# Performance work log

Measured on AMD Instinct MI355X. Metric: run time of the kernel, lower is better.

Reference implementation:

```python
import jax, jax.numpy as jnp
import numpy as np

N = 100000
E = 1600000
F_IN, HID, N_CLS = 128, 16, 32


def setup_inputs() -> dict:
    key = jax.random.key(0)
    ks = jax.random.split(key, 10)
    x = jax.random.normal(ks[0], (N, F_IN), dtype=jnp.float32)
    edge_index = jax.random.randint(ks[1], (2, E), 0, N, dtype=jnp.int64)
    edge_weight = jax.random.uniform(ks[2], (E,), dtype=jnp.float32)
    def glorot(k, shape):
        lim = np.sqrt(6.0 / (shape[0] + shape[1])).astype(np.float32)
        return jax.random.uniform(k, shape, dtype=jnp.float32, minval=-lim, maxval=lim)
    return {
        'x': x, 'edge_index': edge_index, 'edge_weight': edge_weight,
        'W1_0': glorot(ks[3], (F_IN, HID)), 'W1_1': glorot(ks[4], (F_IN, HID)),
        'b1': jnp.zeros((HID,), jnp.float32),
        'W2_0': glorot(ks[5], (HID, N_CLS)), 'W2_1': glorot(ks[6], (HID, N_CLS)),
        'b2': jnp.zeros((N_CLS,), jnp.float32),
    }


def _cheb_conv_k2(x, row, col, edge_weight, W0, W1, b):
    # PyG ChebConv, K=2, lambda_max=2.0:
    #   T0 = x; T1 = L_hat x = D^{-1/2} A D^{-1/2} x - x
    n = x.shape[0]
    deg = jax.ops.segment_sum(edge_weight, row, num_segments=n)  # [N]
    dinv = jnp.where(deg > 0, jax.lax.rsqrt(deg), 0.0)
    norm = dinv[row] * edge_weight * dinv[col]                   # [E]
    agg = jax.ops.segment_sum(norm[:, None] * x[col], row, num_segments=n)  # [N,F]
    tx1 = agg - x
    return x @ W0 + tx1 @ W1 + b


def reference(x, edge_index, edge_weight, W1_0, W1_1, b1, W2_0, W2_1, b2):
    row, col = edge_index[0], edge_index[1]
    h = jax.nn.relu(_cheb_conv_k2(x, row, col, edge_weight, W1_0, W1_1, b1))
    # dropout(p=0) and DFA layers are identity in forward
    out = _cheb_conv_k2(h, row, col, edge_weight, W2_0, W2_1, b2)
    return jax.nn.log_softmax(out, axis=1)
```

## Files before the change

kernel.cpp:

```cpp
#include <hip/hip_runtime.h>
#include <hip/hip_bf16.h>


#include <hip/hip_fp16.h>

constexpr int NN   = 100000;
constexpr int NE   = 1600000;
constexpr int FIN  = 128;
constexpr int HID  = 16;
constexpr int NCLS = 32;

constexpr int RB    = 256;
constexpr int NBKT  = (NN + RB - 1) / RB;
constexpr int EPB   = 4096;
constexpr int EPT   = EPB / 256;
constexpr int GP    = (NE + EPB - 1) / EPB;
constexpr int CAP   = 8192;
constexpr int NTILE = NN / 16;
constexpr int NPAIR = NN / 2;

typedef float f32x2 __attribute__((ext_vector_type(2)));
typedef float f32x4 __attribute__((ext_vector_type(4)));
typedef short bf16x8 __attribute__((ext_vector_type(8)));

#if defined(__has_builtin)
#if __has_builtin(__builtin_amdgcn_cvt_pk_f32_fp8)
#define HAVE_CVT_FP8 1
#endif
#endif

static __device__ __forceinline__ unsigned int f2e4m3(float f) {
    union { float f; unsigned int u; } v; v.f = f;
    unsigned int s = (v.u >> 24) & 0x80u;
    unsigned int au = v.u & 0x7fffffffu;
    if (au > 0x43E00000u) au = 0x43E00000u;
    au += 0x7ffffu + ((au >> 20) & 1u);
    int e4 = (int)(au >> 23) - 120;
    unsigned int m = (au >> 20) & 7u;
    unsigned int byte = (e4 <= 0) ? 0u : (((unsigned int)e4 << 3) | m);
    return s | byte;
}
static __device__ __forceinline__ void fp8x4_fma(unsigned int v, float w, float* acc) {
#ifdef HAVE_CVT_FP8
    f32x2 lo = __builtin_amdgcn_cvt_pk_f32_fp8((int)v, false);
    f32x2 hi = __builtin_amdgcn_cvt_pk_f32_fp8((int)v, true);
    acc[0] += w * lo.x; acc[1] += w * lo.y;
    acc[2] += w * hi.x; acc[3] += w * hi.y;
#else
#pragma unroll
    for (int i = 0; i < 4; i++) {
        unsigned int b = (v >> (8 * i)) & 0xffu;
        float f = __int_as_float((int)(((b & 0x80u) << 24) | ((b & 0x7fu) << 20))) * 0x1p120f;
        acc[i] += w * f;
    }
#endif
}
static __device__ __forceinline__ unsigned short f2bf(float f) {
    union { float f; unsigned int u; } v; v.f = f;
    unsigned int r = v.u + 0x7fffu + ((v.u >> 16) & 1u);
    return (unsigned short)(r >> 16);
}
static __device__ __forceinline__ float bf2f(unsigned short b) {
    union { unsigned int u; float f; } v; v.u = ((unsigned int)b) << 16;
    return v.f;
}
static __device__ __forceinline__ unsigned int wpack(float wf) {
    unsigned int b = __float_as_uint(wf) + 0x8000u;
    return (b >> 16) & 0x7fffu;
}
static __device__ __forceinline__ float wdec(unsigned int u) {
    return __uint_as_float((u >> 17) << 16);
}

__global__ void k_zero_cur(int* __restrict__ bucketCursor) {
    int i = blockIdx.x * blockDim.x + threadIdx.x;
    if (i < NBKT) bucketCursor[i] = 0;
}

__global__ __launch_bounds__(256) void k_partition(
    const int* __restrict__ row, const int* __restrict__ col,
    const float* __restrict__ w, int* __restrict__ bucketCursor,
    int2* __restrict__ partS) {
    __shared__ int2 stage[EPB];
    __shared__ unsigned short sbkt[EPB];
    __shared__ int cnt[NBKT];
    __shared__ int lofs[NBKT];
    __shared__ int cursor[NBKT];
    __shared__ int gbase[NBKT];
    __shared__ int sa[512], sb[512];
    int tid = threadIdx.x;
    long ebase = (long)blockIdx.x * EPB;
    int rr[EPT]; int cc[EPT]; float wv[EPT];
#pragma unroll
    for (int i = 0; i < EPT; i++) {
        long e = ebase + i * 256 + tid;
        if (e < NE) { rr[i] = row[e]; cc[i] = col[e]; wv[i] = w[e]; }
        else rr[i] = -1;
    }
    for (int i = tid; i < NBKT; i += 256) cnt[i] = 0;
    __syncthreads();
#pragma unroll
    for (int i = 0; i < EPT; i++)
        if (rr[i] >= 0) atomicAdd(&cnt[rr[i] >> 8], 1);
    __syncthreads();
    for (int i = tid; i < 512; i += 256) sa[i] = (i < NBKT) ? cnt[i] : 0;
    __syncthreads();
    int* src = sa; int* dst = sb;
    for (int off = 1; off < 512; off <<= 1) {
        for (int i = tid; i < 512; i += 256)
            dst[i] = src[i] + ((i >= off) ? src[i - off] : 0);
        __syncthreads();
        int* t = src; src = dst; dst = t;
    }
    for (int i = tid; i < NBKT; i += 256) {
        int ex = src[i] - cnt[i];
        lofs[i] = ex;
        cursor[i] = ex;
        int go = (cnt[i] > 0) ? atomicAdd(&bucketCursor[i], cnt[i]) : 0;
        gbase[i] = i * CAP + go;
    }
    __syncthreads();
#pragma unroll
    for (int i = 0; i < EPT; i++) {
        if (rr[i] >= 0) {
            int b = rr[i] >> 8;
            int p = atomicAdd(&cursor[b], 1);
            int2 v;
            v.x = cc[i] | ((rr[i] & 255) << 17);
            v.y = __float_as_int(wv[i]);
            stage[p] = v;
            sbkt[p] = (unsigned short)b;
        }
    }
    __syncthreads();
    int total = (int)min((long)EPB, NE - ebase);
    for (int i = tid; i < total; i += 256) {
        int b = sbkt[i];
        partS[gbase[b] + (i - lofs[b])] = stage[i];
    }
}

__global__ __launch_bounds__(256) void k_bucket_sort(
    const int2* __restrict__ partS, const int* __restrict__ bucketCursor,
    unsigned int* __restrict__ partC, int* __restrict__ rowptr,
    float* __restrict__ dinv) {
    __shared__ int hist[RB];
    __shared__ int cursor[RB];
    __shared__ float dsum[RB];
    __shared__ int wtot[4];
    __shared__ int red[4];
    int b = blockIdx.x;
    int tid = threadIdx.x;
    int lane = tid & 63, wv = tid >> 6;
    int partial = 0;
    for (int i = tid; i < b; i += 256) partial += bucketCursor[i];
#pragma unroll
    for (int off = 1; off < 64; off <<= 1) partial += __shfl_xor(partial, off, 64);
    if (lane == 0) red[wv] = partial;
    hist[tid] = 0;
    dsum[tid] = 0.f;
    __syncthreads();
    int start = red[0] + red[1] + red[2] + red[3];
    int count = bucketCursor[b];
    const int2* src = partS + (long)b * CAP;
    for (int i = tid; i < count; i += 256)
        atomicAdd(&hist[((unsigned)src[i].x >> 17) & 255], 1);
    __syncthreads();
    int v = hist[tid];
    int sc = v;
#pragma unroll
    for (int off = 1; off < 64; off <<= 1) {
        int up = __shfl_up(sc, off, 64);
        if (lane >= off) sc += up;
    }
    if (lane == 63) wtot[wv] = sc;
    __syncthreads();
    int add = 0;
    for (int w2 = 0; w2 < wv; w2++) add += wtot[w2];
    int ex = sc + add - v;
    int node = b * RB + tid;
    if (node <= NN) rowptr[node] = start + ex;
    cursor[tid] = ex;
    __syncthreads();
    for (int i = tid; i < count; i += 256) {
        int2 p = src[i];
        int rl = ((unsigned)p.x >> 17) & 255;
        int pos = atomicAdd(&cursor[rl], 1);
        float wf = __int_as_float(p.y);
        partC[start + pos] = ((unsigned)p.x & 0x1FFFFu) | (wpack(wf) << 17);
        atomicAdd(&dsum[rl], wf);
    }
    __syncthreads();
    if (node < NN) {
        float dsv = dsum[tid];
        dinv[node] = dsv > 0.f ? rsqrtf(dsv) : 0.f;
    }
}

__global__ __launch_bounds__(256) void k_proj1(
    const float* __restrict__ x, const float* __restrict__ W0,
    const float* __restrict__ W1, const float* __restrict__ b1,
    const float* __restrict__ dinv,
    float* __restrict__ xa, unsigned char* __restrict__ xb8) {
    int wid = (int)(((long)blockIdx.x * 256 + threadIdx.x) >> 6);
    if (wid >= NTILE) return;
    int lane = threadIdx.x & 63;
    int col = lane & 15, quad = lane >> 4;

    bf16x8 bfrag[2][4];
#pragma unroll
    for (int mat = 0; mat < 2; mat++) {
        const float* W = mat ? W1 : W0;
#pragma unroll
        for (int kb = 0; kb < 4; kb++) {
            bf16x8 f;
#pragma unroll
            for (int j = 0; j < 8; j++)
                f[j] = (short)f2bf(W[(kb * 32 + quad * 8 + j) * HID + col]);
            bfrag[mat][kb] = f;
        }
    }

    const float* xrow = x + ((long)wid * 16 + col) * FIN + quad * 8;
    float4 xb[8];
#pragma unroll
    for (int kb = 0; kb < 4; kb++) {
        xb[2 * kb]     = *(const float4*)(xrow + kb * 32);
        xb[2 * kb + 1] = *(const float4*)(xrow + kb * 32 + 4);
    }
    f32x4 acc0 = {0.f, 0.f, 0.f, 0.f}, acc1 = {0.f, 0.f, 0.f, 0.f};
#pragma unroll
    for (int kb = 0; kb < 4; kb++) {
        float4 a0 = xb[2 * kb], a1 = xb[2 * kb + 1];
        bf16x8 af;
        af[0] = (short)f2bf(a0.x); af[1] = (short)f2bf(a0.y);
        af[2] = (short)f2bf(a0.z); af[3] = (short)f2bf(a0.w);
        af[4] = (short)f2bf(a1.x); af[5] = (short)f2bf(a1.y);
        af[6] = (short)f2bf(a1.z); af[7] = (short)f2bf(a1.w);
        acc0 = __builtin_amdgcn_mfma_f32_16x16x32_bf16(af, bfrag[0][kb], acc0, 0, 0, 0);
        acc1 = __builtin_amdgcn_mfma_f32_16x16x32_bf16(af, bfrag[1][kb], acc1, 0, 0, 0);
    }

    float b1v = b1[col];
#pragma unroll
    for (int r = 0; r < 4; r++) {
        long node = (long)wid * 16 + quad * 4 + r;
        float a0 = acc0[r], a1 = acc1[r];
        xa[node * HID + col] = a0 - a1 + b1v;
        float dn = dinv[node];
        xb8[node * HID + col] = (unsigned char)f2e4m3(dn * a1);
    }
}

__global__ __launch_bounds__(256) void k_gather1(
    const int* __restrict__ rowptr, const unsigned int* __restrict__ partC,
    const float* __restrict__ dinv, const unsigned char* __restrict__ xb8,
    const float* __restrict__ xa,
    unsigned short* __restrict__ h16, unsigned char* __restrict__ h8) {
    long t = (long)blockIdx.x * 256 + threadIdx.x;
    int w = (int)(t >> 6);
    if (w >= NPAIR) return;
    int lane = threadIdx.x & 63;
    int d = lane & 3, p = lane >> 2;
    long n0 = (long)w * 2, n1 = n0 + 1;

    int s0 = rowptr[n0], e0 = rowptr[n0 + 1], e1 = rowptr[n0 + 2];
    float2 dnv = *(const float2*)(dinv + n0);
    float4 xav0 = *(const float4*)(xa + n0 * HID + d * 4);
    float4 xav1 = *(const float4*)(xa + n1 * HID + d * 4);

    float acc0[4] = {0.f, 0.f, 0.f, 0.f};
    float acc1[4] = {0.f, 0.f, 0.f, 0.f};
    int j0 = s0 + p, j1 = e0 + p;
    while ((j0 < e0) | (j1 < e1)) {
        if (j0 < e0) {
            unsigned int u = partC[j0];
            unsigned int v = *(const unsigned int*)(xb8 + (u & 0x1FFFF) * HID + d * 4);
            fp8x4_fma(v, wdec(u), acc0);
            j0 += 16;
        }
        if (j1 < e1) {
            unsigned int u = partC[j1];
            unsigned int v = *(const unsigned int*)(xb8 + (u & 0x1FFFF) * HID + d * 4);
            fp8x4_fma(v, wdec(u), acc1);
            j1 += 16;
        }
    }
#pragma unroll
    for (int i = 0; i < 4; i++) {
        acc0[i] += __shfl_xor(acc0[i], 4);  acc1[i] += __shfl_xor(acc1[i], 4);
        acc0[i] += __shfl_xor(acc0[i], 8);  acc1[i] += __shfl_xor(acc1[i], 8);
        acc0[i] += __shfl_xor(acc0[i], 16); acc1[i] += __shfl_xor(acc1[i], 16);
        acc0[i] += __shfl_xor(acc0[i], 32); acc1[i] += __shfl_xor(acc1[i], 32);
    }
    if (p == 0) {
        float h0[4], h1[4];
        h0[0] = fmaxf(xav0.x + dnv.x * acc0[0], 0.f);
        h0[1] = fmaxf(xav0.y + dnv.x * acc0[1], 0.f);
        h0[2] = fmaxf(xav0.z + dnv.x * acc0[2], 0.f);
        h0[3] = fmaxf(xav0.w + dnv.x * acc0[3], 0.f);
        h1[0] = fmaxf(xav1.x + dnv.y * acc1[0], 0.f);
        h1[1] = fmaxf(xav1.y + dnv.y * acc1[1], 0.f);
        h1[2] = fmaxf(xav1.z + dnv.y * acc1[2], 0.f);
        h1[3] = fmaxf(xav1.w + dnv.y * acc1[3], 0.f);
        ushort4 u0, u1;
        u0.x = f2bf(h0[0]); u0.y = f2bf(h0[1]); u0.z = f2bf(h0[2]); u0.w = f2bf(h0[3]);
        u1.x = f2bf(h1[0]); u1.y = f2bf(h1[1]); u1.z = f2bf(h1[2]); u1.w = f2bf(h1[3]);
        *(ushort4*)(h16 + n0 * HID + d * 4) = u0;
        *(ushort4*)(h16 + n1 * HID + d * 4) = u1;
        unsigned int p0 = f2e4m3(dnv.x * h0[0]) | (f2e4m3(dnv.x * h0[1]) << 8)
                        | (f2e4m3(dnv.x * h0[2]) << 16) | (f2e4m3(dnv.x * h0[3]) << 24);
        unsigned int p1 = f2e4m3(dnv.y * h1[0]) | (f2e4m3(dnv.y * h1[1]) << 8)
                        | (f2e4m3(dnv.y * h1[2]) << 16) | (f2e4m3(dnv.y * h1[3]) << 24);
        *(unsigned int*)(h8 + n0 * HID + d * 4) = p0;
        *(unsigned int*)(h8 + n1 * HID + d * 4) = p1;
    }
}

__global__ __launch_bounds__(256) void k_gather2(
    const int* __restrict__ rowptr, const unsigned int* __restrict__ partC,
    const float* __restrict__ dinv, const unsigned char* __restrict__ h8,
    unsigned short* __restrict__ g16) {
    long t = (long)blockIdx.x * 256 + threadIdx.x;
    int w = (int)(t >> 6);
    if (w >= NPAIR) return;
    int lane = threadIdx.x & 63;
    int d = lane & 3, p = lane >> 2;
    long n0 = (long)w * 2, n1 = n0 + 1;

    int s0 = rowptr[n0], e0 = rowptr[n0 + 1], e1 = rowptr[n0 + 2];
    float2 dnv = *(const float2*)(dinv + n0);

    float acc0[4] = {0.f, 0.f, 0.f, 0.f};
    float acc1[4] = {0.f, 0.f, 0.f, 0.f};
    int j0 = s0 + p, j1 = e0 + p;
    while ((j0 < e0) | (j1 < e1)) {
        if (j0 < e0) {
            unsigned int u = partC[j0];
            unsigned int v = *(const unsigned int*)(h8 + (u & 0x1FFFF) * HID + d * 4);
            fp8x4_fma(v, wdec(u), acc0);
            j0 += 16;
        }
        if (j1 < e1) {
            unsigned int u = partC[j1];
            unsigned int v = *(const unsigned int*)(h8 + (u & 0x1FFFF) * HID + d * 4);
            fp8x4_fma(v, wdec(u), acc1);
            j1 += 16;
        }
    }
#pragma unroll
    for (int i = 0; i < 4; i++) {
        acc0[i] += __shfl_xor(acc0[i], 4);  acc1[i] += __shfl_xor(acc1[i], 4);
        acc0[i] += __shfl_xor(acc0[i], 8);  acc1[i] += __shfl_xor(acc1[i], 8);
        acc0[i] += __shfl_xor(acc0[i], 16); acc1[i] += __shfl_xor(acc1[i], 16);
        acc0[i] += __shfl_xor(acc0[i], 32); acc1[i] += __shfl_xor(acc1[i], 32);
    }
    if (p == 0) {
        ushort4 u0, u1;
        u0.x = f2bf(dnv.x * acc0[0]); u0.y = f2bf(dnv.x * acc0[1]);
        u0.z = f2bf(dnv.x * acc0[2]); u0.w = f2bf(dnv.x * acc0[3]);
        u1.x = f2bf(dnv.y * acc1[0]); u1.y = f2bf(dnv.y * acc1[1]);
        u1.z = f2bf(dnv.y * acc1[2]); u1.w = f2bf(dnv.y * acc1[3]);
        *(ushort4*)(g16 + n0 * HID + d * 4) = u0;
        *(ushort4*)(g16 + n1 * HID + d * 4) = u1;
    }
}

__global__ __launch_bounds__(256) void k_lsm(
    const unsigned short* __restrict__ h16, const unsigned short* __restrict__ g16,
    const float* __restrict__ W0, const float* __restrict__ W1,
    const float* __restrict__ b2, float* __restrict__ out) {
    int wid = (int)(((long)blockIdx.x * 256 + threadIdx.x) >> 6);
    if (wid >= NTILE) return;
    int lane = threadIdx.x & 63;
    int col = lane & 15, quad = lane >> 4;

    bf16x8 bfrag[2];
#pragma unroll
    for (int c = 0; c < 2; c++) {
        bf16x8 f;
        if (quad < 2) {
#pragma unroll
            for (int j = 0; j < 8; j++) {
                int k = quad * 8 + j;
                f[j] = (short)f2bf(W0[k * NCLS + col + 16 * c] - W1[k * NCLS + col + 16 * c]);
            }
        } else {
#pragma unroll
            for (int j = 0; j < 8; j++) {
                int k = (quad - 2) * 8 + j;
                f[j] = (short)f2bf(W1[k * NCLS + col + 16 * c]);
            }
        }
        bfrag[c] = f;
    }

    long node_a = (long)wid * 16 + col;
    const unsigned short* abase =
        (quad & 2) ? (g16 + node_a * HID + (quad & 1) * 8)
                   : (h16 + node_a * HID + (quad & 1) * 8);
    bf16x8 af = *(const bf16x8*)abase;

    f32x4 c0 = {0.f, 0.f, 0.f, 0.f}, c1 = {0.f, 0.f, 0.f, 0.f};
    c0 = __builtin_amdgcn_mfma_f32_16x16x32_bf16(af, bfrag[0], c0, 0, 0, 0);
    c1 = __builtin_amdgcn_mfma_f32_16x16x32_bf16(af, bfrag[1], c1, 0, 0, 0);

    float b2a = b2[col], b2b = b2[col + 16];
#pragma unroll
    for (int r = 0; r < 4; r++) {
        long node = (long)wid * 16 + quad * 4 + r;
        float v0 = c0[r] + b2a;
        float v1 = c1[r] + b2b;
        float m = fmaxf(v0, v1);
        m = fmaxf(m, __shfl_xor(m, 1));
        m = fmaxf(m, __shfl_xor(m, 2));
        m = fmaxf(m, __shfl_xor(m, 4));
        m = fmaxf(m, __shfl_xor(m, 8));
        float sum = __expf(v0 - m) + __expf(v1 - m);
        sum += __shfl_xor(sum, 1);
        sum += __shfl_xor(sum, 2);
        sum += __shfl_xor(sum, 4);
        sum += __shfl_xor(sum, 8);
        float ls = logf(sum);
        out[node * NCLS + col] = v0 - m - ls;
        out[node * NCLS + col + 16] = v1 - m - ls;
    }
}

extern "C" void kernel_launch(void* const* d_in, const int* in_sizes, int n_in,
                              void* d_out, int out_size, void* d_ws, size_t ws_size,
                              hipStream_t stream) {
    const float* x    = (const float*)d_in[0];
    const int*   ei   = (const int*)d_in[1];
    const float* ew   = (const float*)d_in[2];
    const float* W1_0 = (const float*)d_in[3];
    const float* W1_1 = (const float*)d_in[4];
    const float* b1   = (const float*)d_in[5];
    const float* W2_0 = (const float*)d_in[6];
    const float* W2_1 = (const float*)d_in[7];
    const float* b2   = (const float*)d_in[8];
    float* out = (float*)d_out;

    const int* row = ei;
    const int* col = ei + NE;

    char* ws = (char*)d_ws;
    int2*  partS     = (int2*)ws;                 ws += sizeof(int2) * (long)NBKT * CAP;
    unsigned int* partC = (unsigned int*)ws;      ws += sizeof(int) * NE;
    int*   bucketCursor = (int*)ws;               ws += sizeof(int) * NBKT;
    int*   rowptr    = (int*)ws;                  ws += sizeof(int) * (NN + 4);
    float* dinv      = (float*)ws;                ws += sizeof(float) * NN;
    float* xa        = (float*)ws;                ws += sizeof(float) * NN * HID;
    unsigned short* h16 = (unsigned short*)ws;    ws += sizeof(short) * NN * HID;
    unsigned short* g16 = (unsigned short*)ws;    ws += sizeof(short) * NN * HID;
    unsigned char* xb8 = (unsigned char*)ws;      ws += sizeof(char) * NN * HID;
    unsigned char* h8  = (unsigned char*)ws;      ws += sizeof(char) * NN * HID;

    k_zero_cur<<<(NBKT + 255) / 256, 256, 0, stream>>>(bucketCursor);
    k_partition<<<GP, 256, 0, stream>>>(row, col, ew, bucketCursor, partS);
    k_bucket_sort<<<NBKT, 256, 0, stream>>>(partS, bucketCursor, partC, rowptr, dinv);
    k_proj1<<<(NTILE * 64 + 255) / 256, 256, 0, stream>>>(x, W1_0, W1_1, b1, dinv, xa, xb8);
    {
        long th = (long)NPAIR * 64;
        k_gather1<<<(int)((th + 255) / 256), 256, 0, stream>>>(
            rowptr, partC, dinv, xb8, xa, h16, h8);
        k_gather2<<<(int)((th + 255) / 256), 256, 0, stream>>>(
            rowptr, partC, dinv, h8, g16);
    }
    k_lsm<<<(NTILE * 64 + 255) / 256, 256, 0, stream>>>(h16, g16, W2_0, W2_1, b2, out);
}
```

Baseline: 213.8 us.

## Fuse all GCN stages into one cooperative persistent kernel with grid syncs

Replaces the seven separate kernel launches with one cooperative kernel whose stages are separated by grid.sync(). Projection, gather and log-softmax stages become grid-stride loops over persistent waves, and the gather loops prefetch the next pair's rowptr/dinv. The partition stage drops its shared-memory staging and prefix scan and scatters straight to global memory through per-bucket local cursors. The aims are to cut launch overhead and inter-kernel gaps. The costs are grid-wide barriers, a grid capped by occupancy, and shared-memory arrays sized for every stage, which may lower occupancy.

```diff
diff --git a/kernel.cpp b/kernel.cpp
--- a/kernel.cpp
+++ b/kernel.cpp
@@ -1,8 +1,10 @@
 #include <hip/hip_runtime.h>
+#include <hip/hip_cooperative_groups.h>
 #include <hip/hip_bf16.h>
-
-
 #include <hip/hip_fp16.h>
+
+
+namespace cg = cooperative_groups;
 
 constexpr int NN   = 100000;
 constexpr int NE   = 1600000;
@@ -60,10 +62,6 @@
     unsigned int r = v.u + 0x7fffu + ((v.u >> 16) & 1u);
     return (unsigned short)(r >> 16);
 }
-static __device__ __forceinline__ float bf2f(unsigned short b) {
-    union { unsigned int u; float f; } v; v.u = ((unsigned int)b) << 16;
-    return v.f;
-}
 static __device__ __forceinline__ unsigned int wpack(float wf) {
     unsigned int b = __float_as_uint(wf) + 0x8000u;
     return (b >> 16) & 0x7fffu;
@@ -72,358 +70,342 @@
     return __uint_as_float((u >> 17) << 16);
 }
 
-__global__ void k_zero_cur(int* __restrict__ bucketCursor) {
-    int i = blockIdx.x * blockDim.x + threadIdx.x;
-    if (i < NBKT) bucketCursor[i] = 0;
-}
-
-__global__ __launch_bounds__(256) void k_partition(
-    const int* __restrict__ row, const int* __restrict__ col,
-    const float* __restrict__ w, int* __restrict__ bucketCursor,
-    int2* __restrict__ partS) {
-    __shared__ int2 stage[EPB];
-    __shared__ unsigned short sbkt[EPB];
-    __shared__ int cnt[NBKT];
-    __shared__ int lofs[NBKT];
-    __shared__ int cursor[NBKT];
-    __shared__ int gbase[NBKT];
-    __shared__ int sa[512], sb[512];
-    int tid = threadIdx.x;
-    long ebase = (long)blockIdx.x * EPB;
-    int rr[EPT]; int cc[EPT]; float wv[EPT];
-#pragma unroll
-    for (int i = 0; i < EPT; i++) {
-        long e = ebase + i * 256 + tid;
-        if (e < NE) { rr[i] = row[e]; cc[i] = col[e]; wv[i] = w[e]; }
-        else rr[i] = -1;
-    }
-    for (int i = tid; i < NBKT; i += 256) cnt[i] = 0;
-    __syncthreads();
-#pragma unroll
-    for (int i = 0; i < EPT; i++)
-        if (rr[i] >= 0) atomicAdd(&cnt[rr[i] >> 8], 1);
-    __syncthreads();
-    for (int i = tid; i < 512; i += 256) sa[i] = (i < NBKT) ? cnt[i] : 0;
-    __syncthreads();
-    int* src = sa; int* dst = sb;
-    for (int off = 1; off < 512; off <<= 1) {
-        for (int i = tid; i < 512; i += 256)
-            dst[i] = src[i] + ((i >= off) ? src[i - off] : 0);
-        __syncthreads();
-        int* t = src; src = dst; dst = t;
-    }
-    for (int i = tid; i < NBKT; i += 256) {
-        int ex = src[i] - cnt[i];
-        lofs[i] = ex;
-        cursor[i] = ex;
-        int go = (cnt[i] > 0) ? atomicAdd(&bucketCursor[i], cnt[i]) : 0;
-        gbase[i] = i * CAP + go;
-    }
-    __syncthreads();
-#pragma unroll
-    for (int i = 0; i < EPT; i++) {
-        if (rr[i] >= 0) {
-            int b = rr[i] >> 8;
-            int p = atomicAdd(&cursor[b], 1);
-            int2 v;
-            v.x = cc[i] | ((rr[i] & 255) << 17);
-            v.y = __float_as_int(wv[i]);
-            stage[p] = v;
-            sbkt[p] = (unsigned short)b;
-        }
-    }
-    __syncthreads();
-    int total = (int)min((long)EPB, NE - ebase);
-    for (int i = tid; i < total; i += 256) {
-        int b = sbkt[i];
-        partS[gbase[b] + (i - lofs[b])] = stage[i];
-    }
-}
-
-__global__ __launch_bounds__(256) void k_bucket_sort(
-    const int2* __restrict__ partS, const int* __restrict__ bucketCursor,
-    unsigned int* __restrict__ partC, int* __restrict__ rowptr,
-    float* __restrict__ dinv) {
-    __shared__ int hist[RB];
-    __shared__ int cursor[RB];
-    __shared__ float dsum[RB];
-    __shared__ int wtot[4];
-    __shared__ int red[4];
-    int b = blockIdx.x;
-    int tid = threadIdx.x;
-    int lane = tid & 63, wv = tid >> 6;
-    int partial = 0;
-    for (int i = tid; i < b; i += 256) partial += bucketCursor[i];
-#pragma unroll
-    for (int off = 1; off < 64; off <<= 1) partial += __shfl_xor(partial, off, 64);
-    if (lane == 0) red[wv] = partial;
-    hist[tid] = 0;
-    dsum[tid] = 0.f;
-    __syncthreads();
-    int start = red[0] + red[1] + red[2] + red[3];
-    int count = bucketCursor[b];
-    const int2* src = partS + (long)b * CAP;
-    for (int i = tid; i < count; i += 256)
-        atomicAdd(&hist[((unsigned)src[i].x >> 17) & 255], 1);
-    __syncthreads();
-    int v = hist[tid];
-    int sc = v;
-#pragma unroll
-    for (int off = 1; off < 64; off <<= 1) {
-        int up = __shfl_up(sc, off, 64);
-        if (lane >= off) sc += up;
-    }
-    if (lane == 63) wtot[wv] = sc;
-    __syncthreads();
-    int add = 0;
-    for (int w2 = 0; w2 < wv; w2++) add += wtot[w2];
-    int ex = sc + add - v;
-    int node = b * RB + tid;
-    if (node <= NN) rowptr[node] = start + ex;
-    cursor[tid] = ex;
-    __syncthreads();
-    for (int i = tid; i < count; i += 256) {
-        int2 p = src[i];
-        int rl = ((unsigned)p.x >> 17) & 255;
-        int pos = atomicAdd(&cursor[rl], 1);
-        float wf = __int_as_float(p.y);
-        partC[start + pos] = ((unsigned)p.x & 0x1FFFFu) | (wpack(wf) << 17);
-        atomicAdd(&dsum[rl], wf);
-    }
-    __syncthreads();
-    if (node < NN) {
-        float dsv = dsum[tid];
-        dinv[node] = dsv > 0.f ? rsqrtf(dsv) : 0.f;
-    }
-}
-
-__global__ __launch_bounds__(256) void k_proj1(
-    const float* __restrict__ x, const float* __restrict__ W0,
-    const float* __restrict__ W1, const float* __restrict__ b1,
-    const float* __restrict__ dinv,
-    float* __restrict__ xa, unsigned char* __restrict__ xb8) {
-    int wid = (int)(((long)blockIdx.x * 256 + threadIdx.x) >> 6);
-    if (wid >= NTILE) return;
-    int lane = threadIdx.x & 63;
-    int col = lane & 15, quad = lane >> 4;
-
-    bf16x8 bfrag[2][4];
-#pragma unroll
-    for (int mat = 0; mat < 2; mat++) {
-        const float* W = mat ? W1 : W0;
-#pragma unroll
-        for (int kb = 0; kb < 4; kb++) {
+__global__ __launch_bounds__(256, 4) void k_mega(
+    const float* __restrict__ x, const int* __restrict__ row,
+    const int* __restrict__ col, const float* __restrict__ ew,
+    const float* __restrict__ W1_0, const float* __restrict__ W1_1,
+    const float* __restrict__ b1,
+    const float* __restrict__ W2_0, const float* __restrict__ W2_1,
+    const float* __restrict__ b2, float* __restrict__ out,
+    int2* __restrict__ partS, unsigned int* __restrict__ partC,
+    int* __restrict__ bucketCursor, int* __restrict__ rowptr,
+    float* __restrict__ dinv, float* __restrict__ xa,
+    unsigned short* __restrict__ h16, unsigned short* __restrict__ g16,
+    unsigned char* __restrict__ xb8, unsigned char* __restrict__ h8) {
+    cg::grid_group grid = cg::this_grid();
+    int bid = blockIdx.x, tid = threadIdx.x;
+    int lane = tid & 63;
+    int TW = (int)(gridDim.x << 2);
+    int gw = (bid << 2) | (tid >> 6);
+
+    __shared__ int sh_cnt[NBKT];
+    __shared__ int sh_gbase[NBKT];
+    __shared__ int sh_lcur[NBKT];
+    __shared__ int sh_hist[RB];
+    __shared__ int sh_cursor[RB];
+    __shared__ float sh_dsum[RB];
+    __shared__ int sh_wtot[4];
+    __shared__ int sh_red[4];
+
+    for (int i = bid * 256 + tid; i < NBKT; i += (int)gridDim.x * 256)
+        bucketCursor[i] = 0;
+    grid.sync();
+
+    if (bid < GP) {
+        long ebase = (long)bid * EPB;
+        int rr[EPT]; int cc[EPT]; float wv[EPT];
+#pragma unroll
+        for (int i = 0; i < EPT; i++) {
+            long e = ebase + i * 256 + tid;
+            if (e < NE) { rr[i] = row[e]; cc[i] = col[e]; wv[i] = ew[e]; }
+            else rr[i] = -1;
+        }
+        for (int i = tid; i < NBKT; i += 256) { sh_cnt[i] = 0; sh_lcur[i] = 0; }
+        __syncthreads();
+#pragma unroll
+        for (int i = 0; i < EPT; i++)
+            if (rr[i] >= 0) atomicAdd(&sh_cnt[rr[i] >> 8], 1);
+        __syncthreads();
+        for (int i = tid; i < NBKT; i += 256) {
+            int c = sh_cnt[i];
+            sh_gbase[i] = i * CAP + ((c > 0) ? atomicAdd(&bucketCursor[i], c) : 0);
+        }
+        __syncthreads();
+#pragma unroll
+        for (int i = 0; i < EPT; i++) {
+            if (rr[i] >= 0) {
+                int b = rr[i] >> 8;
+                int pos = atomicAdd(&sh_lcur[b], 1);
+                int2 v;
+                v.x = cc[i] | ((rr[i] & 255) << 17);
+                v.y = __float_as_int(wv[i]);
+                partS[sh_gbase[b] + pos] = v;
+            }
+        }
+    }
+    grid.sync();
+
+    if (bid < NBKT) {
+        int b = bid;
+        int wv = tid >> 6;
+        int partial = 0;
+        for (int i = tid; i < b; i += 256) partial += bucketCursor[i];
+#pragma unroll
+        for (int off = 1; off < 64; off <<= 1) partial += __shfl_xor(partial, off, 64);
+        if (lane == 0) sh_red[wv] = partial;
+        sh_hist[tid] = 0;
+        sh_dsum[tid] = 0.f;
+        __syncthreads();
+        int start = sh_red[0] + sh_red[1] + sh_red[2] + sh_red[3];
+        int count = bucketCursor[b];
+        const int2* src = partS + (long)b * CAP;
+        for (int i = tid; i < count; i += 256)
+            atomicAdd(&sh_hist[((unsigned)src[i].x >> 17) & 255], 1);
+        __syncthreads();
+        int v = sh_hist[tid];
+        int sc = v;
+#pragma unroll
+        for (int off = 1; off < 64; off <<= 1) {
+            int up = __shfl_up(sc, off, 64);
+            if (lane >= off) sc += up;
+        }
+        if (lane == 63) sh_wtot[wv] = sc;
+        __syncthreads();
+        int add = 0;
+        for (int w2 = 0; w2 < wv; w2++) add += sh_wtot[w2];
+        int ex = sc + add - v;
+        int node = b * RB + tid;
+        if (node <= NN) rowptr[node] = start + ex;
+        sh_cursor[tid] = ex;
+        __syncthreads();
+        for (int i = tid; i < count; i += 256) {
+            int2 p = src[i];
+            int rl = ((unsigned)p.x >> 17) & 255;
+            int pos = atomicAdd(&sh_cursor[rl], 1);
+            float wf = __int_as_float(p.y);
+            partC[start + pos] = ((unsigned)p.x & 0x1FFFFu) | (wpack(wf) << 17);
+            atomicAdd(&sh_dsum[rl], wf);
+        }
+        __syncthreads();
+        if (node < NN) {
+            float dsv = sh_dsum[tid];
+            dinv[node] = dsv > 0.f ? rsqrtf(dsv) : 0.f;
+        }
+    }
+    grid.sync();
+
+    {
+        int pcol = lane & 15, quad = lane >> 4;
+        bf16x8 bfrag[2][4];
+#pragma unroll
+        for (int mat = 0; mat < 2; mat++) {
+            const float* W = mat ? W1_1 : W1_0;
+#pragma unroll
+            for (int kb = 0; kb < 4; kb++) {
+                bf16x8 f;
+#pragma unroll
+                for (int j = 0; j < 8; j++)
+                    f[j] = (short)f2bf(W[(kb * 32 + quad * 8 + j) * HID + pcol]);
+                bfrag[mat][kb] = f;
+            }
+        }
+        float b1v = b1[pcol];
+        for (int wid = gw; wid < NTILE; wid += TW) {
+            const float* xrow = x + ((long)wid * 16 + pcol) * FIN + quad * 8;
+            float4 xb[8];
+#pragma unroll
+            for (int kb = 0; kb < 4; kb++) {
+                xb[2 * kb]     = *(const float4*)(xrow + kb * 32);
+                xb[2 * kb + 1] = *(const float4*)(xrow + kb * 32 + 4);
+            }
+            f32x4 acc0 = {0.f, 0.f, 0.f, 0.f}, acc1 = {0.f, 0.f, 0.f, 0.f};
+#pragma unroll
+            for (int kb = 0; kb < 4; kb++) {
+                float4 a0 = xb[2 * kb], a1 = xb[2 * kb + 1];
+                bf16x8 af;
+                af[0] = (short)f2bf(a0.x); af[1] = (short)f2bf(a0.y);
+                af[2] = (short)f2bf(a0.z); af[3] = (short)f2bf(a0.w);
+                af[4] = (short)f2bf(a1.x); af[5] = (short)f2bf(a1.y);
+                af[6] = (short)f2bf(a1.z); af[7] = (short)f2bf(a1.w);
+                acc0 = __builtin_amdgcn_mfma_f32_16x16x32_bf16(af, bfrag[0][kb], acc0, 0, 0, 0);
+                acc1 = __builtin_amdgcn_mfma_f32_16x16x32_bf16(af, bfrag[1][kb], acc1, 0, 0, 0);
+            }
+#pragma unroll
+            for (int r = 0; r < 4; r++) {
+                long node = (long)wid * 16 + quad * 4 + r;
+                float a0 = acc0[r], a1 = acc1[r];
+                xa[node * HID + pcol] = a0 - a1 + b1v;
+                float dn = dinv[node];
+                xb8[node * HID + pcol] = (unsigned char)f2e4m3(dn * a1);
+            }
+        }
+    }
+    grid.sync();
+
+    {
+        int d = lane & 3, p = lane >> 2;
+        int pr = gw;
+        int s0 = 0, e0 = 0, e1 = 0; float2 dnv = {0.f, 0.f};
+        if (pr < NPAIR) {
+            s0 = rowptr[2 * pr]; e0 = rowptr[2 * pr + 1]; e1 = rowptr[2 * pr + 2];
+            dnv = *(const float2*)(dinv + 2 * pr);
+        }
+        while (pr < NPAIR) {
+            int np = pr + TW;
+            int s0n = 0, e0n = 0, e1n = 0; float2 dnvn = {0.f, 0.f};
+            if (np < NPAIR) {
+                s0n = rowptr[2 * np]; e0n = rowptr[2 * np + 1]; e1n = rowptr[2 * np + 2];
+                dnvn = *(const float2*)(dinv + 2 * np);
+            }
+            long n0 = (long)pr * 2, n1 = n0 + 1;
+            float4 xav0 = *(const float4*)(xa + n0 * HID + d * 4);
+            float4 xav1 = *(const float4*)(xa + n1 * HID + d * 4);
+            float acc0[4] = {0.f, 0.f, 0.f, 0.f};
+            float acc1[4] = {0.f, 0.f, 0.f, 0.f};
+            int j0 = s0 + p, j1 = e0 + p;
+            while ((j0 < e0) | (j1 < e1)) {
+                if (j0 < e0) {
+                    unsigned int u = partC[j0];
+                    unsigned int v = *(const unsigned int*)(xb8 + (u & 0x1FFFF) * HID + d * 4);
+                    fp8x4_fma(v, wdec(u), acc0);
+                    j0 += 16;
+                }
+                if (j1 < e1) {
+                    unsigned int u = partC[j1];
+                    unsigned int v = *(const unsigned int*)(xb8 + (u & 0x1FFFF) * HID + d * 4);
+                    fp8x4_fma(v, wdec(u), acc1);
+                    j1 += 16;
+                }
+            }
+#pragma unroll
+            for (int i = 0; i < 4; i++) {
+                acc0[i] += __shfl_xor(acc0[i], 4);  acc1[i] += __shfl_xor(acc1[i], 4);
+                acc0[i] += __shfl_xor(acc0[i], 8);  acc1[i] += __shfl_xor(acc1[i], 8);
+                acc0[i] += __shfl_xor(acc0[i], 16); acc1[i] += __shfl_xor(acc1[i], 16);
+                acc0[i] += __shfl_xor(acc0[i], 32); acc1[i] += __shfl_xor(acc1[i], 32);
+            }
+            if (p == 0) {
+                float h0[4], h1[4];
+                h0[0] = fmaxf(xav0.x + dnv.x * acc0[0], 0.f);
+                h0[1] = fmaxf(xav0.y + dnv.x * acc0[1], 0.f);
+                h0[2] = fmaxf(xav0.z + dnv.x * acc0[2], 0.f);
+                h0[3] = fmaxf(xav0.w + dnv.x * acc0[3], 0.f);
+                h1[0] = fmaxf(xav1.x + dnv.y * acc1[0], 0.f);
+                h1[1] = fmaxf(xav1.y + dnv.y * acc1[1], 0.f);
+                h1[2] = fmaxf(xav1.z + dnv.y * acc1[2], 0.f);
+                h1[3] = fmaxf(xav1.w + dnv.y * acc1[3], 0.f);
+                ushort4 u0, u1;
+                u0.x = f2bf(h0[0]); u0.y = f2bf(h0[1]); u0.z = f2bf(h0[2]); u0.w = f2bf(h0[3]);
+                u1.x = f2bf(h1[0]); u1.y = f2bf(h1[1]); u1.z = f2bf(h1[2]); u1.w = f2bf(h1[3]);
+                *(ushort4*)(h16 + n0 * HID + d * 4) = u0;
+                *(ushort4*)(h16 + n1 * HID + d * 4) = u1;
+                unsigned int p0 = f2e4m3(dnv.x * h0[0]) | (f2e4m3(dnv.x * h0[1]) << 8)
+                                | (f2e4m3(dnv.x * h0[2]) << 16) | (f2e4m3(dnv.x * h0[3]) << 24);
+                unsigned int p1 = f2e4m3(dnv.y * h1[0]) | (f2e4m3(dnv.y * h1[1]) << 8)
+                                | (f2e4m3(dnv.y * h1[2]) << 16) | (f2e4m3(dnv.y * h1[3]) << 24);
+                *(unsigned int*)(h8 + n0 * HID + d * 4) = p0;
+                *(unsigned int*)(h8 + n1 * HID + d * 4) = p1;
+            }
+            pr = np; s0 = s0n; e0 = e0n; e1 = e1n; dnv = dnvn;
+        }
+    }
+    grid.sync();
+
+    {
+        int d = lane & 3, p = lane >> 2;
+        int pr = gw;
+        int s0 = 0, e0 = 0, e1 = 0; float2 dnv = {0.f, 0.f};
+        if (pr < NPAIR) {
+            s0 = rowptr[2 * pr]; e0 = rowptr[2 * pr + 1]; e1 = rowptr[2 * pr + 2];
+            dnv = *(const float2*)(dinv + 2 * pr);
+        }
+        while (pr < NPAIR) {
+            int np = pr + TW;
+            int s0n = 0, e0n = 0, e1n = 0; float2 dnvn = {0.f, 0.f};
+            if (np < NPAIR) {
+                s0n = rowptr[2 * np]; e0n = rowptr[2 * np + 1]; e1n = rowptr[2 * np + 2];
+                dnvn = *(const float2*)(dinv + 2 * np);
+            }
+            long n0 = (long)pr * 2, n1 = n0 + 1;
+            float acc0[4] = {0.f, 0.f, 0.f, 0.f};
+            float acc1[4] = {0.f, 0.f, 0.f, 0.f};
+            int j0 = s0 + p, j1 = e0 + p;
+            while ((j0 < e0) | (j1 < e1)) {
+                if (j0 < e0) {
+                    unsigned int u = partC[j0];
+                    unsigned int v = *(const unsigned int*)(h8 + (u & 0x1FFFF) * HID + d * 4);
+                    fp8x4_fma(v, wdec(u), acc0);
+                    j0 += 16;
+                }
+                if (j1 < e1) {
+                    unsigned int u = partC[j1];
+                    unsigned int v = *(const unsigned int*)(h8 + (u & 0x1FFFF) * HID + d * 4);
+                    fp8x4_fma(v, wdec(u), acc1);
+                    j1 += 16;
+                }
+            }
+#pragma unroll
+            for (int i = 0; i < 4; i++) {
+                acc0[i] += __shfl_xor(acc0[i], 4);  acc1[i] += __shfl_xor(acc1[i], 4);
+                acc0[i] += __shfl_xor(acc0[i], 8);  acc1[i] += __shfl_xor(acc1[i], 8);
+                acc0[i] += __shfl_xor(acc0[i], 16); acc1[i] += __shfl_xor(acc1[i], 16);
+                acc0[i] += __shfl_xor(acc0[i], 32); acc1[i] += __shfl_xor(acc1[i], 32);
+            }
+            if (p == 0) {
+                ushort4 u0, u1;
+                u0.x = f2bf(dnv.x * acc0[0]); u0.y = f2bf(dnv.x * acc0[1]);
+                u0.z = f2bf(dnv.x * acc0[2]); u0.w = f2bf(dnv.x * acc0[3]);
+                u1.x = f2bf(dnv.y * acc1[0]); u1.y = f2bf(dnv.y * acc1[1]);
+                u1.z = f2bf(dnv.y * acc1[2]); u1.w = f2bf(dnv.y * acc1[3]);
+                *(ushort4*)(g16 + n0 * HID + d * 4) = u0;
+                *(ushort4*)(g16 + n1 * HID + d * 4) = u1;
+            }
+            pr = np; s0 = s0n; e0 = e0n; e1 = e1n; dnv = dnvn;
+        }
+    }
+    grid.sync();
+
+    {
+        int pcol = lane & 15, quad = lane >> 4;
+        bf16x8 bfrag[2];
+#pragma unroll
+        for (int c = 0; c < 2; c++) {
             bf16x8 f;
-#pragma unroll
-            for (int j = 0; j < 8; j++)
-                f[j] = (short)f2bf(W[(kb * 32 + quad * 8 + j) * HID + col]);
-            bfrag[mat][kb] = f;
-        }
-    }
-
-    const float* xrow = x + ((long)wid * 16 + col) * FIN + quad * 8;
-    float4 xb[8];
-#pragma unroll
-    for (int kb = 0; kb < 4; kb++) {
-        xb[2 * kb]     = *(const float4*)(xrow + kb * 32);
-        xb[2 * kb + 1] = *(const float4*)(xrow + kb * 32 + 4);
-    }
-    f32x4 acc0 = {0.f, 0.f, 0.f, 0.f}, acc1 = {0.f, 0.f, 0.f, 0.f};
-#pragma unroll
-    for (int kb = 0; kb < 4; kb++) {
-        float4 a0 = xb[2 * kb], a1 = xb[2 * kb + 1];
-        bf16x8 af;
-        af[0] = (short)f2bf(a0.x); af[1] = (short)f2bf(a0.y);
-        af[2] = (short)f2bf(a0.z); af[3] = (short)f2bf(a0.w);
-        af[4] = (short)f2bf(a1.x); af[5] = (short)f2bf(a1.y);
-        af[6] = (short)f2bf(a1.z); af[7] = (short)f2bf(a1.w);
-        acc0 = __builtin_amdgcn_mfma_f32_16x16x32_bf16(af, bfrag[0][kb], acc0, 0, 0, 0);
-        acc1 = __builtin_amdgcn_mfma_f32_16x16x32_bf16(af, bfrag[1][kb], acc1, 0, 0, 0);
-    }
-
-    float b1v = b1[col];
-#pragma unroll
-    for (int r = 0; r < 4; r++) {
-        long node = (long)wid * 16 + quad * 4 + r;
-        float a0 = acc0[r], a1 = acc1[r];
-        xa[node * HID + col] = a0 - a1 + b1v;
-        float dn = dinv[node];
-        xb8[node * HID + col] = (unsigned char)f2e4m3(dn * a1);
-    }
-}
-
-__global__ __launch_bounds__(256) void k_gather1(
-    const int* __restrict__ rowptr, const unsigned int* __restrict__ partC,
-    const float* __restrict__ dinv, const unsigned char* __restrict__ xb8,
-    const float* __restrict__ xa,
-    unsigned short* __restrict__ h16, unsigned char* __restrict__ h8) {
-    long t = (long)blockIdx.x * 256 + threadIdx.x;
-    int w = (int)(t >> 6);
-    if (w >= NPAIR) return;
-    int lane = threadIdx.x & 63;
-    int d = lane & 3, p = lane >> 2;
-    long n0 = (long)w * 2, n1 = n0 + 1;
-
-    int s0 = rowptr[n0], e0 = rowptr[n0 + 1], e1 = rowptr[n0 + 2];
-    float2 dnv = *(const float2*)(dinv + n0);
-    float4 xav0 = *(const float4*)(xa + n0 * HID + d * 4);
-    float4 xav1 = *(const float4*)(xa + n1 * HID + d * 4);
-
-    float acc0[4] = {0.f, 0.f, 0.f, 0.f};
-    float acc1[4] = {0.f, 0.f, 0.f, 0.f};
-    int j0 = s0 + p, j1 = e0 + p;
-    while ((j0 < e0) | (j1 < e1)) {
-        if (j0 < e0) {
-            unsigned int u = partC[j0];
-            unsigned int v = *(const unsigned int*)(xb8 + (u & 0x1FFFF) * HID + d * 4);
-            fp8x4_fma(v, wdec(u), acc0);
-            j0 += 16;
-        }
-        if (j1 < e1) {
-            unsigned int u = partC[j1];
-            unsigned int v = *(const unsigned int*)(xb8 + (u & 0x1FFFF) * HID + d * 4);
-            fp8x4_fma(v, wdec(u), acc1);
-            j1 += 16;
-        }
-    }
-#pragma unroll
-    for (int i = 0; i < 4; i++) {
-        acc0[i] += __shfl_xor(acc0[i], 4);  acc1[i] += __shfl_xor(acc1[i], 4);
-        acc0[i] += __shfl_xor(acc0[i], 8);  acc1[i] += __shfl_xor(acc1[i], 8);
-        acc0[i] += __shfl_xor(acc0[i], 16); acc1[i] += __shfl_xor(acc1[i], 16);
-        acc0[i] += __shfl_xor(acc0[i], 32); acc1[i] += __shfl_xor(acc1[i], 32);
-    }
-    if (p == 0) {
-        float h0[4], h1[4];
-        h0[0] = fmaxf(xav0.x + dnv.x * acc0[0], 0.f);
-        h0[1] = fmaxf(xav0.y + dnv.x * acc0[1], 0.f);
-        h0[2] = fmaxf(xav0.z + dnv.x * acc0[2], 0.f);
-        h0[3] = fmaxf(xav0.w + dnv.x * acc0[3], 0.f);
-        h1[0] = fmaxf(xav1.x + dnv.y * acc1[0], 0.f);
-        h1[1] = fmaxf(xav1.y + dnv.y * acc1[1], 0.f);
-        h1[2] = fmaxf(xav1.z + dnv.y * acc1[2], 0.f);
-        h1[3] = fmaxf(xav1.w + dnv.y * acc1[3], 0.f);
-        ushort4 u0, u1;
-        u0.x = f2bf(h0[0]); u0.y = f2bf(h0[1]); u0.z = f2bf(h0[2]); u0.w = f2bf(h0[3]);
-        u1.x = f2bf(h1[0]); u1.y = f2bf(h1[1]); u1.z = f2bf(h1[2]); u1.w = f2bf(h1[3]);
-        *(ushort4*)(h16 + n0 * HID + d * 4) = u0;
-        *(ushort4*)(h16 + n1 * HID + d * 4) = u1;
-        unsigned int p0 = f2e4m3(dnv.x * h0[0]) | (f2e4m3(dnv.x * h0[1]) << 8)
-                        | (f2e4m3(dnv.x * h0[2]) << 16) | (f2e4m3(dnv.x * h0[3]) << 24);
-        unsigned int p1 = f2e4m3(dnv.y * h1[0]) | (f2e4m3(dnv.y * h1[1]) << 8)
-                        | (f2e4m3(dnv.y * h1[2]) << 16) | (f2e4m3(dnv.y * h1[3]) << 24);
-        *(unsigned int*)(h8 + n0 * HID + d * 4) = p0;
-        *(unsigned int*)(h8 + n1 * HID + d * 4) = p1;
-    }
-}
-
-__global__ __launch_bounds__(256) void k_gather2(
-    const int* __restrict__ rowptr, const unsigned int* __restrict__ partC,
-    const float* __restrict__ dinv, const unsigned char* __restrict__ h8,
-    unsigned short* __restrict__ g16) {
-    long t = (long)blockIdx.x * 256 + threadIdx.x;
-    int w = (int)(t >> 6);
-    if (w >= NPAIR) return;
-    int lane = threadIdx.x & 63;
-    int d = lane & 3, p = lane >> 2;
-    long n0 = (long)w * 2, n1 = n0 + 1;
-
-    int s0 = rowptr[n0], e0 = rowptr[n0 + 1], e1 = rowptr[n0 + 2];
-    float2 dnv = *(const float2*)(dinv + n0);
-
-    float acc0[4] = {0.f, 0.f, 0.f, 0.f};
-    float acc1[4] = {0.f, 0.f, 0.f, 0.f};
-    int j0 = s0 + p, j1 = e0 + p;
-    while ((j0 < e0) | (j1 < e1)) {
-        if (j0 < e0) {
-            unsigned int u = partC[j0];
-            unsigned int v = *(const unsigned int*)(h8 + (u & 0x1FFFF) * HID + d * 4);
-            fp8x4_fma(v, wdec(u), acc0);
-            j0 += 16;
-        }
-        if (j1 < e1) {
-            unsigned int u = partC[j1];
-            unsigned int v = *(const unsigned int*)(h8 + (u & 0x1FFFF) * HID + d * 4);
-            fp8x4_fma(v, wdec(u), acc1);
-            j1 += 16;
-        }
-    }
-#pragma unroll
-    for (int i = 0; i < 4; i++) {
-        acc0[i] += __shfl_xor(acc0[i], 4);  acc1[i] += __shfl_xor(acc1[i], 4);
-        acc0[i] += __shfl_xor(acc0[i], 8);  acc1[i] += __shfl_xor(acc1[i], 8);
-        acc0[i] += __shfl_xor(acc0[i], 16); acc1[i] += __shfl_xor(acc1[i], 16);
-        acc0[i] += __shfl_xor(acc0[i], 32); acc1[i] += __shfl_xor(acc1[i], 32);
-    }
-    if (p == 0) {
-        ushort4 u0, u1;
-        u0.x = f2bf(dnv.x * acc0[0]); u0.y = f2bf(dnv.x * acc0[1]);
-        u0.z = f2bf(dnv.x * acc0[2]); u0.w = f2bf(dnv.x * acc0[3]);
-        u1.x = f2bf(dnv.y * acc1[0]); u1.y = f2bf(dnv.y * acc1[1]);
-        u1.z = f2bf(dnv.y * acc1[2]); u1.w = f2bf(dnv.y * acc1[3]);
-        *(ushort4*)(g16 + n0 * HID + d * 4) = u0;
-        *(ushort4*)(g16 + n1 * HID + d * 4) = u1;
-    }
-}
-
-__global__ __launch_bounds__(256) void k_lsm(
-    const unsigned short* __restrict__ h16, const unsigned short* __restrict__ g16,
-    const float* __restrict__ W0, const float* __restrict__ W1,
-    const float* __restrict__ b2, float* __restrict__ out) {
-    int wid = (int)(((long)blockIdx.x * 256 + threadIdx.x) >> 6);
-    if (wid >= NTILE) return;
-    int lane = threadIdx.x & 63;
-    int col = lane & 15, quad = lane >> 4;
-
-    bf16x8 bfrag[2];
-#pragma unroll
-    for (int c = 0; c < 2; c++) {
-        bf16x8 f;
-        if (quad < 2) {
-#pragma unroll
-            for (int j = 0; j < 8; j++) {
-                int k = quad * 8 + j;
-                f[j] = (short)f2bf(W0[k * NCLS + col + 16 * c] - W1[k * NCLS + col + 16 * c]);
-            }
-        } else {
-#pragma unroll
-            for (int j = 0; j < 8; j++) {
-                int k = (quad - 2) * 8 + j;
-                f[j] = (short)f2bf(W1[k * NCLS + col + 16 * c]);
-            }
-        }
-        bfrag[c] = f;
-    }
-
-    long node_a = (long)wid * 16 + col;
-    const unsigned short* abase =
-        (quad & 2) ? (g16 + node_a * HID + (quad & 1) * 8)
-                   : (h16 + node_a * HID + (quad & 1) * 8);
-    bf16x8 af = *(const bf16x8*)abase;
-
-    f32x4 c0 = {0.f, 0.f, 0.f, 0.f}, c1 = {0.f, 0.f, 0.f, 0.f};
-    c0 = __builtin_amdgcn_mfma_f32_16x16x32_bf16(af, bfrag[0], c0, 0, 0, 0);
-    c1 = __builtin_amdgcn_mfma_f32_16x16x32_bf16(af, bfrag[1], c1, 0, 0, 0);
-
-    float b2a = b2[col], b2b = b2[col + 16];
-#pragma unroll
-    for (int r = 0; r < 4; r++) {
-        long node = (long)wid * 16 + quad * 4 + r;
-        float v0 = c0[r] + b2a;
-        float v1 = c1[r] + b2b;
-        float m = fmaxf(v0, v1);
-        m = fmaxf(m, __shfl_xor(m, 1));
-        m = fmaxf(m, __shfl_xor(m, 2));
-        m = fmaxf(m, __shfl_xor(m, 4));
-        m = fmaxf(m, __shfl_xor(m, 8));
-        float sum = __expf(v0 - m) + __expf(v1 - m);
-        sum += __shfl_xor(sum, 1);
-        sum += __shfl_xor(sum, 2);
-        sum += __shfl_xor(sum, 4);
-        sum += __shfl_xor(sum, 8);
-        float ls = logf(sum);
-        out[node * NCLS + col] = v0 - m - ls;
-        out[node * NCLS + col + 16] = v1 - m - ls;
+            if (quad < 2) {
+#pragma unroll
+                for (int j = 0; j < 8; j++) {
+                    int k = quad * 8 + j;
+                    f[j] = (short)f2bf(W2_0[k * NCLS + pcol + 16 * c] - W2_1[k * NCLS + pcol + 16 * c]);
+                }
+            } else {
+#pragma unroll
+                for (int j = 0; j < 8; j++) {
+                    int k = (quad - 2) * 8 + j;
+                    f[j] = (short)f2bf(W2_1[k * NCLS + pcol + 16 * c]);
+                }
+            }
+            bfrag[c] = f;
+        }
+        float b2a = b2[pcol], b2b = b2[pcol + 16];
+        for (int wid = gw; wid < NTILE; wid += TW) {
+            long node_a = (long)wid * 16 + pcol;
+            const unsigned short* abase =
+                (quad & 2) ? (g16 + node_a * HID + (quad & 1) * 8)
+                           : (h16 + node_a * HID + (quad & 1) * 8);
+            bf16x8 af = *(const bf16x8*)abase;
+            f32x4 c0 = {0.f, 0.f, 0.f, 0.f}, c1 = {0.f, 0.f, 0.f, 0.f};
+            c0 = __builtin_amdgcn_mfma_f32_16x16x32_bf16(af, bfrag[0], c0, 0, 0, 0);
+            c1 = __builtin_amdgcn_mfma_f32_16x16x32_bf16(af, bfrag[1], c1, 0, 0, 0);
+#pragma unroll
+            for (int r = 0; r < 4; r++) {
+                long node = (long)wid * 16 + quad * 4 + r;
+                float v0 = c0[r] + b2a;
+                float v1 = c1[r] + b2b;
+                float m = fmaxf(v0, v1);
+                m = fmaxf(m, __shfl_xor(m, 1));
+                m = fmaxf(m, __shfl_xor(m, 2));
+                m = fmaxf(m, __shfl_xor(m, 4));
+                m = fmaxf(m, __shfl_xor(m, 8));
+                float sum = __expf(v0 - m) + __expf(v1 - m);
+                sum += __shfl_xor(sum, 1);
+                sum += __shfl_xor(sum, 2);
+                sum += __shfl_xor(sum, 4);
+                sum += __shfl_xor(sum, 8);
+                float ls = logf(sum);
+                out[node * NCLS + pcol] = v0 - m - ls;
+                out[node * NCLS + pcol + 16] = v1 - m - ls;
+            }
+        }
     }
 }
 
@@ -456,16 +438,30 @@
     unsigned char* xb8 = (unsigned char*)ws;      ws += sizeof(char) * NN * HID;
     unsigned char* h8  = (unsigned char*)ws;      ws += sizeof(char) * NN * HID;
 
-    k_zero_cur<<<(NBKT + 255) / 256, 256, 0, stream>>>(bucketCursor);
-    k_partition<<<GP, 256, 0, stream>>>(row, col, ew, bucketCursor, partS);
-    k_bucket_sort<<<NBKT, 256, 0, stream>>>(partS, bucketCursor, partC, rowptr, dinv);
-    k_proj1<<<(NTILE * 64 + 255) / 256, 256, 0, stream>>>(x, W1_0, W1_1, b1, dinv, xa, xb8);
-    {
-        long th = (long)NPAIR * 64;
-        k_gather1<<<(int)((th + 255) / 256), 256, 0, stream>>>(
-            rowptr, partC, dinv, xb8, xa, h16, h8);
-        k_gather2<<<(int)((th + 255) / 256), 256, 0, stream>>>(
-            rowptr, partC, dinv, h8, g16);
-    }
-    k_lsm<<<(NTILE * 64 + 255) / 256, 256, 0, stream>>>(h16, g16, W2_0, W2_1, b2, out);
-}
+    static int s_grid = 0;
+    if (s_grid == 0) {
+        int occ = 0;
+        hipError_t err = hipOccupancyMaxActiveBlocksPerMultiprocessor(&occ, k_mega, 256, 0);
+        int ncu = 256;
+        hipDeviceProp_t prop;
+        int dev = 0;
+        if (hipGetDevice(&dev) == hipSuccess &&
+            hipGetDeviceProperties(&prop, dev) == hipSuccess)
+            ncu = prop.multiProcessorCount;
+        long g = (err == hipSuccess && occ > 0) ? (long)occ * ncu : 1024;
+        if (g > 2048) g = 2048;
+        if (g < GP) g = GP;
+        s_grid = (int)g;
+    }
+
+    void* kargs[] = {
+        (void*)&x, (void*)&row, (void*)&col, (void*)&ew,
+        (void*)&W1_0, (void*)&W1_1, (void*)&b1,
+        (void*)&W2_0, (void*)&W2_1, (void*)&b2, (void*)&out,
+        (void*)&partS, (void*)&partC, (void*)&bucketCursor, (void*)&rowptr,
+        (void*)&dinv, (void*)&xa, (void*)&h16, (void*)&g16,
+        (void*)&xb8, (void*)&h8
+    };
+    hipLaunchCooperativeKernel((void*)k_mega, dim3(s_grid), dim3(256),
+                               kargs, 0, stream);
+}
```

Result: slower. 642.3 us (+200.4%).
